# Optimization experiments

Hardware: AMD Instinct MI355X
Metric: run time of the kernel (lower is better)

Reference implementation:

```python
import jax, jax.numpy as jnp
import numpy as np
from jax import lax

N = 512  # neurons (== input features in this base class)

@jax.custom_vjp
def spike_fn(x):
    # Heaviside spike with fast-sigmoid surrogate gradient (standard for LIF SNNs)
    return (x > 0.0).astype(x.dtype)

def _spike_fwd(x):
    return spike_fn(x), x

def _spike_bwd(x, g):
    sg = 1.0 / (1.0 + 10.0 * jnp.abs(x)) ** 2
    return (g * sg,)

spike_fn.defvjp(_spike_fwd, _spike_bwd)

def setup_inputs() -> dict:
    key = jax.random.key(0)
    k1, k2, k3, k4, k5, k6 = jax.random.split(key, 6)
    B, T = 64, 1000
    scale = 1.0 / np.sqrt(N)
    return {
        "input_batch": jax.random.normal(k1, (B, T, N), dtype=jnp.float32),
        "state_snn": jnp.zeros((2, B, N), dtype=jnp.float32),  # [v; s]
        "state_LI": jnp.zeros((B, N), dtype=jnp.float32),
        "W1": jax.random.normal(k2, (N, N), dtype=jnp.float32) * scale,
        "W2": jax.random.normal(k3, (N, N), dtype=jnp.float32) * scale,
        "leak_v": jax.random.uniform(k4, (N,), dtype=jnp.float32, minval=0.8, maxval=0.99),
        "leak_i": jax.random.uniform(k5, (N,), dtype=jnp.float32, minval=0.8, maxval=0.99),
        "thresh": jax.random.uniform(k6, (N,), dtype=jnp.float32, minval=0.5, maxval=1.5),
    }

def reference(input_batch, state_snn, state_LI, W1, W2, leak_v, leak_i, thresh):
    # input_batch: [B, T, N]; time loop expressed as lax.scan over T
    v0, s0 = state_snn[0], state_snn[1]
    xs = jnp.swapaxes(input_batch, 0, 1)  # [T, B, N]

    def step(carry, x_t):
        v, s, u = carry
        ff = x_t @ W1.T                        # LIF feed-forward current
        v = leak_v * v * (1.0 - s) + ff        # leak + reset-to-zero on spike
        s = spike_fn(v - thresh)               # spike generation
        u = leak_i * u + s @ W2.T              # leaky-integrator readout
        return (v, s, u), (s, jnp.stack([v, s]), u)

    _, (spikes, states_snn, decoded) = lax.scan(step, (v0, s0, state_LI), xs)
    # spikes: [T,B,N], states_snn: [T,2,B,N], decoded: [T,B,N]
    return spikes, states_snn, decoded
```

## Files before the change

kernel.cpp:

```cpp
#include <hip/hip_runtime.h>

#define T_STEPS 1000
#define B_SZ 64
#define N_SZ 512
#define BN_TOT (B_SZ * N_SZ)
#define TBN   ((size_t)T_STEPS * BN_TOT)

typedef __attribute__((ext_vector_type(4))) float f32x4;
typedef __attribute__((ext_vector_type(8))) short bf16x8;
typedef unsigned short ushort_t;

__global__ __launch_bounds__(256, 4)
void sgemm_abt(const float* __restrict__ A, const float* __restrict__ W,
               float* __restrict__ C)
{
    constexpr int K = 512;
    constexpr int BK = 16;
    constexpr int LDT = 128 + 4;
    __shared__ float As[BK][LDT];
    __shared__ float Bs[BK][LDT];

    const int tid = threadIdx.x;
    const int tx = tid & 15;
    const int ty = tid >> 4;
    const size_t m0 = (size_t)blockIdx.y * 128;
    const int n0 = blockIdx.x * 128;

    float acc[8][8];
#pragma unroll
    for (int i = 0; i < 8; ++i)
#pragma unroll
        for (int j = 0; j < 8; ++j) acc[i][j] = 0.0f;

    for (int k0 = 0; k0 < K; k0 += BK) {
#pragma unroll
        for (int p = 0; p < 2; ++p) {
            int i = tid + p * 256;
            int r = i >> 2;
            int q = i & 3;
            float4 va = *(const float4*)(A + (m0 + r) * K + k0 + q * 4);
            As[q * 4 + 0][r] = va.x; As[q * 4 + 1][r] = va.y;
            As[q * 4 + 2][r] = va.z; As[q * 4 + 3][r] = va.w;
            float4 vb = *(const float4*)(W + (size_t)(n0 + r) * K + k0 + q * 4);
            Bs[q * 4 + 0][r] = vb.x; Bs[q * 4 + 1][r] = vb.y;
            Bs[q * 4 + 2][r] = vb.z; Bs[q * 4 + 3][r] = vb.w;
        }
        __syncthreads();
#pragma unroll
        for (int k = 0; k < BK; ++k) {
            float a[8], b[8];
            *(float4*)&a[0] = *(const float4*)&As[k][ty * 8];
            *(float4*)&a[4] = *(const float4*)&As[k][ty * 8 + 4];
            *(float4*)&b[0] = *(const float4*)&Bs[k][tx * 4];
            *(float4*)&b[4] = *(const float4*)&Bs[k][tx * 4 + 64];
#pragma unroll
            for (int i = 0; i < 8; ++i)
#pragma unroll
                for (int j = 0; j < 8; ++j)
                    acc[i][j] = fmaf(a[i], b[j], acc[i][j]);
        }
        __syncthreads();
    }

#pragma unroll
    for (int i = 0; i < 8; ++i) {
        float* cp = C + (m0 + ty * 8 + i) * 512 + n0 + tx * 4;
        *(float4*)cp        = make_float4(acc[i][0], acc[i][1], acc[i][2], acc[i][3]);
        *(float4*)(cp + 64) = make_float4(acc[i][4], acc[i][5], acc[i][6], acc[i][7]);
    }
}

__global__ __launch_bounds__(256)
void w2_split(const float* __restrict__ W2, ushort_t* __restrict__ Wc)
{
    int i = blockIdx.x * 256 + threadIdx.x;
    int n = i >> 9, k = i & 511;
    float w = W2[i];
    unsigned wb = __float_as_uint(w);
    float h = __uint_as_float(wb & 0xFFFF0000u);
    float r1 = w - h;
    unsigned r1b = __float_as_uint(r1);
    size_t base = (size_t)n * 1024 + k;
    Wc[base]       = (ushort_t)(wb >> 16);
    Wc[base + 512] = (ushort_t)(r1b >> 16);
}

__device__ __forceinline__ uint4 mexp8(unsigned bb)
{
    uint4 r;
    r.x = ((bb) & 1u) * 0x3F80u        | (((bb) >> 1) & 1u) * 0x3F800000u;
    r.y = (((bb) >> 2) & 1u) * 0x3F80u | (((bb) >> 3) & 1u) * 0x3F800000u;
    r.z = (((bb) >> 4) & 1u) * 0x3F80u | (((bb) >> 5) & 1u) * 0x3F800000u;
    r.w = (((bb) >> 6) & 1u) * 0x3F80u | (((bb) >> 7) & 1u) * 0x3F800000u;
    return r;
}

__global__ __launch_bounds__(256, 2)
void gemm2_mfma(const unsigned* __restrict__ Msk, const ushort_t* __restrict__ Wc,
                float* __restrict__ C)
{
    constexpr int NT = 1024 / 32;
    __shared__ ushort_t As[2][128 * 32];
    __shared__ ushort_t Bs[2][128 * 32];

    const int tid = threadIdx.x;
    const int m0 = blockIdx.y * 128;
    const int n0 = blockIdx.x * 128;
    const int wid = tid >> 6;
    const int lane = tid & 63;
    const int wm = (wid >> 1) * 64;
    const int wn = (wid & 1) * 64;
    const int fr = lane & 15;
    const int fq = lane >> 4;

    f32x4 acc[4][4] = {};

    const int rA = tid >> 2;
    const int cA = (tid & 3) * 8;
    const size_t mrow0 = (size_t)(m0 + (tid >> 2)) * 16;
    const size_t mrow1 = (size_t)(m0 + 64 + (tid >> 2)) * 16;
    const int qsh = (tid & 3) * 8;

    unsigned mw0, mw1;

#define STAGE_B(buf, t)                                                      \
    {                                                                        \
        const int k0_ = (t) * 32;                                            \
        _Pragma("unroll")                                                    \
        for (int i = 0; i < 2; ++i) {                                        \
            __builtin_amdgcn_global_load_lds(                                \
                (const __attribute__((address_space(1))) unsigned int*)      \
                    (Wc + (size_t)(n0 + i * 64 + rA) * 1024 + k0_ + cA),     \
                (__attribute__((address_space(3))) unsigned int*)            \
                    (Bs[buf] + i * 2048 + tid * 8),                          \
                16, 0, 0);                                                   \
        }                                                                    \
    }
#define MLOAD(t)                                                             \
    {                                                                        \
        const int kk_ = ((t) * 32) & 511;       \
        mw0 = Msk[mrow0 + (kk_ >> 5)];                                       \
        mw1 = Msk[mrow1 + (kk_ >> 5)];                                       \
    }
#define MSTORE(buf)                                                          \
    {                                                                        \
        *(uint4*)(As[buf] + tid * 8)        = mexp8((mw0 >> qsh) & 0xFFu);   \
        *(uint4*)(As[buf] + 2048 + tid * 8) = mexp8((mw1 >> qsh) & 0xFFu);   \
    }

    MLOAD(0);
    STAGE_B(0, 0);
    MSTORE(0);
    asm volatile("s_waitcnt vmcnt(0)" ::: "memory");
    __syncthreads();

    int cur = 0;
    for (int t = 0; t < NT; ++t) {
        if (t + 1 < NT) {
            MLOAD(t + 1);
            STAGE_B(cur ^ 1, t + 1);
        }

        bf16x8 a[4], b[4];
#pragma unroll
        for (int m = 0; m < 4; ++m)
            a[m] = *(const bf16x8*)(As[cur] + (wm + m * 16 + fr) * 32 + fq * 8);
#pragma unroll
        for (int n = 0; n < 4; ++n)
            b[n] = *(const bf16x8*)(Bs[cur] + (wn + n * 16 + fr) * 32 + fq * 8);
#pragma unroll
        for (int m = 0; m < 4; ++m)
#pragma unroll
            for (int n = 0; n < 4; ++n)
                acc[m][n] = __builtin_amdgcn_mfma_f32_16x16x32_bf16(
                    a[m], b[n], acc[m][n], 0, 0, 0);

        if (t + 1 < NT)
            MSTORE(cur ^ 1);

        asm volatile("s_waitcnt vmcnt(0)" ::: "memory");
        __syncthreads();
        cur ^= 1;
    }
#undef STAGE_B
#undef MLOAD
#undef MSTORE

#pragma unroll
    for (int m = 0; m < 4; ++m) {
        const int row = m0 + wm + m * 16 + fq * 4;
#pragma unroll
        for (int n = 0; n < 4; ++n) {
            const int col = n0 + wn + n * 16 + fr;
#pragma unroll
            for (int j = 0; j < 4; ++j)
                C[(size_t)(row + j) * 512 + col] = acc[m][n][j];
        }
    }
}

__global__ __launch_bounds__(128)
void lif_scan(const float* __restrict__ ff, const float* __restrict__ st0,
              const float* __restrict__ leak_v, const float* __restrict__ thresh,
              float* __restrict__ spikes, float* __restrict__ states,
              unsigned long long* __restrict__ Msk)
{
    const int idx = blockIdx.x * 128 + threadIdx.x;
    const int n = idx & (N_SZ - 1);
    const int b = idx >> 9;

    float v = st0[idx];
    float s = st0[BN_TOT + idx];
    const float lv = leak_v[n];
    const float th = thresh[n];

    const float* fp = ff + (size_t)b * T_STEPS * N_SZ + n;
    float* sp  = spikes + idx;
    float* stp = states + idx;
    const int wslot = idx >> 6;
    const bool wlead = ((threadIdx.x & 63) == 0);

    float f[8];
#pragma unroll
    for (int j = 0; j < 8; ++j) f[j] = fp[(size_t)j * N_SZ];

    for (int t = 0; t < T_STEPS; t += 8) {
        float g[8];
#pragma unroll
        for (int j = 0; j < 8; ++j) g[j] = 0.f;
        if (t + 8 < T_STEPS) {
            const float* q = fp + (size_t)(t + 8) * N_SZ;
#pragma unroll
            for (int j = 0; j < 8; ++j) g[j] = q[(size_t)j * N_SZ];
        }
#pragma unroll
        for (int j = 0; j < 8; ++j) {
            v = lv * v * (1.0f - s) + f[j];
            s = (v > th) ? 1.0f : 0.0f;
            size_t o  = (size_t)(t + j) * BN_TOT;
            size_t o2 = (size_t)(t + j) * (2 * BN_TOT);
            sp[o] = s;
            stp[o2] = v;
            stp[o2 + BN_TOT] = s;
            unsigned long long bm = __ballot(s != 0.0f);
            if (Msk && wlead)
                Msk[(size_t)(t + j) * 512 + wslot] = bm;
        }
#pragma unroll
        for (int j = 0; j < 8; ++j) f[j] = g[j];
    }
}

__global__ __launch_bounds__(128)
void li_scan(float* __restrict__ dec, const float* __restrict__ u0,
             const float* __restrict__ leak_i)
{
    const int idx = blockIdx.x * 128 + threadIdx.x;
    const int n = idx & (N_SZ - 1);

    float u = u0[idx];
    const float li = leak_i[n];
    float* p = dec + idx;

    float y[8];
#pragma unroll
    for (int j = 0; j < 8; ++j) y[j] = p[(size_t)j * BN_TOT];

    for (int t = 0; t < T_STEPS; t += 8) {
        float g[8];
#pragma unroll
        for (int j = 0; j < 8; ++j) g[j] = 0.f;
        if (t + 8 < T_STEPS) {
            float* q = p + (size_t)(t + 8) * BN_TOT;
#pragma unroll
            for (int j = 0; j < 8; ++j) g[j] = q[(size_t)j * BN_TOT];
        }
#pragma unroll
        for (int j = 0; j < 8; ++j) {
            u = fmaf(li, u, y[j]);
            p[(size_t)(t + j) * BN_TOT] = u;
        }
#pragma unroll
        for (int j = 0; j < 8; ++j) y[j] = g[j];
    }
}

extern "C" void kernel_launch(void* const* d_in, const int* in_sizes, int n_in,
                              void* d_out, int out_size, void* d_ws, size_t ws_size,
                              hipStream_t stream)
{
    (void)in_sizes; (void)n_in; (void)out_size;

    const float* X     = (const float*)d_in[0];
    const float* st_sn = (const float*)d_in[1];
    const float* st_li = (const float*)d_in[2];
    const float* W1    = (const float*)d_in[3];
    const float* W2    = (const float*)d_in[4];
    const float* lv    = (const float*)d_in[5];
    const float* li    = (const float*)d_in[6];
    const float* th    = (const float*)d_in[7];

    float* spikes = (float*)d_out;
    float* states = spikes + TBN;
    float* dec    = states + 2 * TBN;

    const size_t WS_NEED = (size_t)512 * 1024 * 2 + (size_t)1000 * 512 * 8;
    const bool use_mfma = (ws_size >= WS_NEED);
    ushort_t* Wc = (ushort_t*)d_ws;
    unsigned long long* Msk = (unsigned long long*)(Wc + (size_t)512 * 1024);

    const dim3 gemm_grid(4, 500), gemm_block(256);
    const dim3 scan_grid(BN_TOT / 128), scan_block(128);

    if (use_mfma)
        w2_split<<<dim3(1024), dim3(256), 0, stream>>>(W2, Wc);

    sgemm_abt<<<gemm_grid, gemm_block, 0, stream>>>(X, W1, dec);

    lif_scan<<<scan_grid, scan_block, 0, stream>>>(dec, st_sn, lv, th,
                                                   spikes, states,
                                                   use_mfma ? Msk
                                                            : (unsigned long long*)0);

    if (use_mfma)
        gemm2_mfma<<<gemm_grid, gemm_block, 0, stream>>>((const unsigned*)Msk,
                                                         Wc, dec);
    else
        sgemm_abt<<<gemm_grid, gemm_block, 0, stream>>>(spikes, W2, dec);

    li_scan<<<scan_grid, scan_block, 0, stream>>>(dec, st_li, li);
}
```

Before: 732.3 us.

## Drop LDS staging in spike GEMM; load fragments directly from global

Rewrites the gemm2_mfma main loop so that each wave loads its own B fragments from the split-bf16 weights and its own spike-mask words straight from global memory into registers, expanding the mask to bf16 in registers. This removes the shared-memory double buffer, the global_load_lds staging and the per-iteration barriers. Occupancy bounds are raised from 2 to 3 blocks per CU. The trade-off is redundant global and L2 traffic, since waves sharing a tile each reload the same data, and no software prefetch to hide load latency.

```diff
diff --git a/kernel.cpp b/kernel.cpp
--- a/kernel.cpp
+++ b/kernel.cpp
@@ -8,6 +8,7 @@
 
 typedef __attribute__((ext_vector_type(4))) float f32x4;
 typedef __attribute__((ext_vector_type(8))) short bf16x8;
+typedef __attribute__((ext_vector_type(4))) unsigned uint32x4;
 typedef unsigned short ushort_t;
 
 __global__ __launch_bounds__(256, 4)
@@ -85,24 +86,21 @@
     Wc[base + 512] = (ushort_t)(r1b >> 16);
 }
 
-__device__ __forceinline__ uint4 mexp8(unsigned bb)
-{
-    uint4 r;
-    r.x = ((bb) & 1u) * 0x3F80u        | (((bb) >> 1) & 1u) * 0x3F800000u;
-    r.y = (((bb) >> 2) & 1u) * 0x3F80u | (((bb) >> 3) & 1u) * 0x3F800000u;
-    r.z = (((bb) >> 4) & 1u) * 0x3F80u | (((bb) >> 5) & 1u) * 0x3F800000u;
-    r.w = (((bb) >> 6) & 1u) * 0x3F80u | (((bb) >> 7) & 1u) * 0x3F800000u;
-    return r;
-}
-
-__global__ __launch_bounds__(256, 2)
+union bfcast { uint32x4 u; bf16x8 v; };
+__device__ __forceinline__ bf16x8 mexp8v(unsigned bb)
+{
+    bfcast c;
+    c.u.x = (bb & 1u)        * 0x3F80u | ((bb >> 1) & 1u) * 0x3F800000u;
+    c.u.y = ((bb >> 2) & 1u) * 0x3F80u | ((bb >> 3) & 1u) * 0x3F800000u;
+    c.u.z = ((bb >> 4) & 1u) * 0x3F80u | ((bb >> 5) & 1u) * 0x3F800000u;
+    c.u.w = ((bb >> 6) & 1u) * 0x3F80u | ((bb >> 7) & 1u) * 0x3F800000u;
+    return c.v;
+}
+
+__global__ __launch_bounds__(256, 3)
 void gemm2_mfma(const unsigned* __restrict__ Msk, const ushort_t* __restrict__ Wc,
                 float* __restrict__ C)
 {
-    constexpr int NT = 1024 / 32;
-    __shared__ ushort_t As[2][128 * 32];
-    __shared__ ushort_t Bs[2][128 * 32];
-
     const int tid = threadIdx.x;
     const int m0 = blockIdx.y * 128;
     const int n0 = blockIdx.x * 128;
@@ -112,79 +110,42 @@
     const int wn = (wid & 1) * 64;
     const int fr = lane & 15;
     const int fq = lane >> 4;
+    const int qsh = fq * 8;
 
     f32x4 acc[4][4] = {};
 
-    const int rA = tid >> 2;
-    const int cA = (tid & 3) * 8;
-    const size_t mrow0 = (size_t)(m0 + (tid >> 2)) * 16;
-    const size_t mrow1 = (size_t)(m0 + 64 + (tid >> 2)) * 16;
-    const int qsh = (tid & 3) * 8;
-
-    unsigned mw0, mw1;
-
-#define STAGE_B(buf, t)                                                      \
-    {                                                                        \
-        const int k0_ = (t) * 32;                                            \
-        _Pragma("unroll")                                                    \
-        for (int i = 0; i < 2; ++i) {                                        \
-            __builtin_amdgcn_global_load_lds(                                \
-                (const __attribute__((address_space(1))) unsigned int*)      \
-                    (Wc + (size_t)(n0 + i * 64 + rA) * 1024 + k0_ + cA),     \
-                (__attribute__((address_space(3))) unsigned int*)            \
-                    (Bs[buf] + i * 2048 + tid * 8),                          \
-                16, 0, 0);                                                   \
-        }                                                                    \
-    }
-#define MLOAD(t)                                                             \
-    {                                                                        \
-        const int kk_ = ((t) * 32) & 511;       \
-        mw0 = Msk[mrow0 + (kk_ >> 5)];                                       \
-        mw1 = Msk[mrow1 + (kk_ >> 5)];                                       \
-    }
-#define MSTORE(buf)                                                          \
-    {                                                                        \
-        *(uint4*)(As[buf] + tid * 8)        = mexp8((mw0 >> qsh) & 0xFFu);   \
-        *(uint4*)(As[buf] + 2048 + tid * 8) = mexp8((mw1 >> qsh) & 0xFFu);   \
-    }
-
-    MLOAD(0);
-    STAGE_B(0, 0);
-    MSTORE(0);
-    asm volatile("s_waitcnt vmcnt(0)" ::: "memory");
-    __syncthreads();
-
-    int cur = 0;
-    for (int t = 0; t < NT; ++t) {
-        if (t + 1 < NT) {
-            MLOAD(t + 1);
-            STAGE_B(cur ^ 1, t + 1);
-        }
-
-        bf16x8 a[4], b[4];
-#pragma unroll
-        for (int m = 0; m < 4; ++m)
-            a[m] = *(const bf16x8*)(As[cur] + (wm + m * 16 + fr) * 32 + fq * 8);
+    const size_t mrow[4] = {
+        (size_t)(m0 + wm +  0 + fr) * 16, (size_t)(m0 + wm + 16 + fr) * 16,
+        (size_t)(m0 + wm + 32 + fr) * 16, (size_t)(m0 + wm + 48 + fr) * 16 };
+    const size_t brow[4] = {
+        (size_t)(n0 + wn +  0 + fr) * 1024, (size_t)(n0 + wn + 16 + fr) * 1024,
+        (size_t)(n0 + wn + 32 + fr) * 1024, (size_t)(n0 + wn + 48 + fr) * 1024 };
+
+#pragma unroll 1
+    for (int t = 0; t < 32; ++t) {
+        const int k0 = t * 32;
+        const int kk = k0 & 511;
+        const int mword = kk >> 5;
+
+        unsigned mw[4];
+        bf16x8 b[4];
+#pragma unroll
+        for (int m = 0; m < 4; ++m) mw[m] = Msk[mrow[m] + mword];
 #pragma unroll
         for (int n = 0; n < 4; ++n)
-            b[n] = *(const bf16x8*)(Bs[cur] + (wn + n * 16 + fr) * 32 + fq * 8);
+            b[n] = *(const bf16x8*)(Wc + brow[n] + k0 + qsh);
+
+        bf16x8 a[4];
+#pragma unroll
+        for (int m = 0; m < 4; ++m) a[m] = mexp8v((mw[m] >> qsh) & 0xFFu);
+
 #pragma unroll
         for (int m = 0; m < 4; ++m)
 #pragma unroll
             for (int n = 0; n < 4; ++n)
                 acc[m][n] = __builtin_amdgcn_mfma_f32_16x16x32_bf16(
                     a[m], b[n], acc[m][n], 0, 0, 0);
-
-        if (t + 1 < NT)
-            MSTORE(cur ^ 1);
-
-        asm volatile("s_waitcnt vmcnt(0)" ::: "memory");
-        __syncthreads();
-        cur ^= 1;
-    }
-#undef STAGE_B
-#undef MLOAD
-#undef MSTORE
+    }
 
 #pragma unroll
     for (int m = 0; m < 4; ++m) {
```

After: 881.8 us. 20.4% more time.
